# Kernel tuning notes

Hardware: AMD Instinct MI355X
Metric: run time of the kernel (lower is better)

The kernel has to match this reference:

```python
import jax, jax.numpy as jnp
import numpy as np

B, T, N, D, H, E = 64, 64, 32, 32, 128, 256


def setup_inputs() -> dict:
    key = jax.random.key(0)
    ks = jax.random.split(key, 20)

    def g(k, shape, scale=0.1):
        return (jax.random.normal(k, shape, dtype=jnp.float32) * scale)

    return {
        "ts_batch": jax.random.normal(ks[0], (B, T, N, D), dtype=jnp.float32),
        "edge_index": jax.random.randint(ks[1], (2, E), 0, N, dtype=jnp.int32),
        # encoder: 2-layer GCN-LSTM, gates packed as [i,f,g,o] -> 4H
        "Wen0": g(ks[2], (D + H, 4 * H)), "ben0": jnp.zeros((4 * H,), jnp.float32),
        "Wen1": g(ks[3], (2 * H, 4 * H)), "ben1": jnp.zeros((4 * H,), jnp.float32),
        # decoder: 2-layer GCN-LSTM
        "Wde0": g(ks[4], (D + H, 4 * H)), "bde0": jnp.zeros((4 * H,), jnp.float32),
        "Wde1": g(ks[5], (2 * H, 4 * H)), "bde1": jnp.zeros((4 * H,), jnp.float32),
        # per-node linears (the nn.ModuleList loops, batched as [N, in, out])
        "Wmu": g(ks[6], (N, H, H)), "bmu": jnp.zeros((N, H), jnp.float32),
        "Wlv": g(ks[7], (N, H, H)), "blv": jnp.zeros((N, H), jnp.float32),
        "Who": g(ks[8], (N, H, D)), "bho": jnp.zeros((N, D), jnp.float32),
        "Wholv": g(ks[9], (N, H, D)), "bholv": jnp.zeros((N, D), jnp.float32),
        # reparametrization noise (torch.randn_like), made explicit for determinism
        "eps": jax.random.normal(ks[10], (B, N, H), dtype=jnp.float32),
    }


def reference(ts_batch, edge_index, Wen0, ben0, Wen1, ben1, Wde0, bde0, Wde1, bde1,
              Wmu, bmu, Wlv, blv, Who, bho, Wholv, bholv, eps):
    n = Wmu.shape[0]
    # GCN normalized adjacency with self-loops: D^{-1/2}(A+I)D^{-1/2}
    A = jnp.zeros((n, n), jnp.float32).at[edge_index[1], edge_index[0]].add(1.0)
    A = A + jnp.eye(n, dtype=jnp.float32)
    dinv = jax.lax.rsqrt(A.sum(axis=1))
    A = dinv[:, None] * A * dinv[None, :]

    def gcn(x, W, b):  # x: [B,N,F] -> [B,N,4H]
        return jnp.einsum('ij,bjf->bif', A, x) @ W + b

    def cell(x, h, c, W, b):
        z = gcn(jnp.concatenate([x, h], axis=-1), W, b)
        i, f, g, o = jnp.split(z, 4, axis=-1)
        c = jax.nn.sigmoid(f) * c + jax.nn.sigmoid(i) * jnp.tanh(g)
        h = jax.nn.sigmoid(o) * jnp.tanh(c)
        return h, c

    def pnl(x, W, b):  # per-node linear, replaces the python loop over ModuleList
        return jnp.einsum('bnh,nho->bno', x, W) + b

    bsz, tlen = ts_batch.shape[0], ts_batch.shape[1]
    hdim = Wen0.shape[1] // 4
    z0 = jnp.zeros((bsz, n, hdim), jnp.float32)

    def enc_step(carry, x_t):
        h0, c0, h1, c1 = carry
        h0, c0 = cell(x_t, h0, c0, Wen0, ben0)
        h1, c1 = cell(h0, h1, c1, Wen1, ben1)
        return (h0, c0, h1, c1), None

    (h0, c0, h1, c1), _ = jax.lax.scan(
        enc_step, (z0, z0, z0, z0), jnp.transpose(ts_batch, (1, 0, 2, 3)))

    mu = pnl(h1, Wmu, bmu)
    logvar = pnl(h1, Wlv, blv)
    zlat = mu + eps * jnp.exp(logvar)  # reparametrize (note: exp(logvar), as in source)

    out_last = pnl(zlat, Who, bho)
    outlv_last = pnl(zlat, Wholv, bholv)

    # decoder initialized from encoder final (pre-reparam) hidden state; runs in
    # reverse time feeding back its own output (inference / no teacher forcing)
    def dec_step(carry, _):
        h0, c0, h1, c1, prev = carry
        h0, c0 = cell(prev, h0, c0, Wde0, bde0)
        h1, c1 = cell(h0, h1, c1, Wde1, bde1)
        out = pnl(h1, Who, bho)
        outlv = pnl(h1, Wholv, bholv)
        return (h0, c0, h1, c1, out), (out, outlv)

    _, (outs, outlvs) = jax.lax.scan(
        dec_step, (h0, c0, h1, c1, out_last), None, length=tlen - 1)

    # outs are for timesteps T-2 .. 0; reverse and append step T-1
    output = jnp.concatenate([outs[::-1], out_last[None]], axis=0)
    output_logvar = jnp.concatenate([outlvs[::-1], outlv_last[None]], axis=0)
    output = jnp.transpose(output, (1, 0, 2, 3))            # [B,T,N,D]
    output_logvar = jnp.transpose(output_logvar, (1, 0, 2, 3))
    return output, zlat, mu, logvar, output_logvar
```

## Files before the change

kernel.cpp:

```cpp
#include <hip/hip_runtime.h>


typedef unsigned short u16;
typedef unsigned int u32;
typedef short bf16x8 __attribute__((ext_vector_type(8)));
typedef float f32x4 __attribute__((ext_vector_type(4)));

#define O_OUT 0
#define O_Z   4194304
#define O_MU  4456448
#define O_LV  4718592
#define O_OLV 4980736

#define WS_ABF  0
#define WS_PEN0 1280
#define WS_PEN1 83200
#define WS_PDE0 214272
#define WS_PDE1 296192
#define WS_PHO  427264
#define WS_PLV  558336
#define WS_H1   689408
#define WS_NEED_BYTES 34408960ull

#define XSTR 552

__device__ __forceinline__ u16 f2b(float f){
  unsigned x = __float_as_uint(f);
  x += 0x7fffu + ((x>>16)&1u);
  return (u16)(x>>16);
}
__device__ __forceinline__ float b2f(u16 u){ return __uint_as_float(((unsigned)u)<<16); }
__device__ __forceinline__ float blo(unsigned u){ return __uint_as_float(u<<16); }
__device__ __forceinline__ float bhi(unsigned u){ return __uint_as_float(u & 0xffff0000u); }

__device__ __forceinline__ float rcp_(float x){ return __builtin_amdgcn_rcpf(x); }
__device__ __forceinline__ float sigm(float x){ return rcp_(1.f + __expf(-x)); }
__device__ __forceinline__ float tanh_(float x){
  float e = __expf(-2.f*fabsf(x));
  float r = (1.f - e) * rcp_(1.f + e);
  return __builtin_copysignf(r, x);
}

__global__ void adj_kernel(const int* __restrict__ ei, u16* __restrict__ ws)
{
  __shared__ float As[1024];
  __shared__ float dinv[32];
  const int tid = threadIdx.x;
  for (int e = tid; e < 1024; e += 256) As[e] = 0.f;
  __syncthreads();
  atomicAdd(&As[ei[256 + tid]*32 + ei[tid]], 1.f);
  __syncthreads();
  if (tid < 32) As[tid*33] += 1.f;
  __syncthreads();
  if (tid < 32){
    float s = 0.f;
    for (int j=0;j<32;++j) s += As[tid*32 + j];
    dinv[tid] = rsqrtf(s);
  }
  __syncthreads();
  for (int e = tid; e < 1280; e += 256){
    int i = e / 40, j = e % 40;
    float v = (j < 32) ? As[i*32 + j]*dinv[i]*dinv[j] : 0.f;
    ws[WS_ABF + e] = f2b(v);
  }
}

__global__ void pack_kernel(const float* __restrict__ Wen0, const float* __restrict__ Wen1,
                            const float* __restrict__ Wde0, const float* __restrict__ Wde1,
                            const float* __restrict__ Who,  const float* __restrict__ Wholv,
                            u16* __restrict__ ws)
{
  int id = blockIdx.x*256 + threadIdx.x;
  if (id < 53248){
    const float* W; int KS, dstoff, lid;
    if (id < 10240){ W = Wen0; KS = 5; dstoff = WS_PEN0; lid = id; }
    else if (id < 26624){ W = Wen1; KS = 8; dstoff = WS_PEN1; lid = id - 10240; }
    else if (id < 36864){ W = Wde0; KS = 5; dstoff = WS_PDE0; lid = id - 26624; }
    else { W = Wde1; KS = 8; dstoff = WS_PDE1; lid = id - 36864; }
    int l = lid & 63, rest = lid >> 6;
    int ks = rest % KS, nt = rest / KS;
    int n  = nt*16 + (l & 15);
    int k0 = ks*32 + (l >> 4)*8;
    u16 tmp[8];
    #pragma unroll
    for (int j=0;j<8;++j) tmp[j] = f2b(W[(k0 + j)*512 + n]);
    uint4 v;
    v.x = (unsigned)tmp[0] | ((unsigned)tmp[1] << 16);
    v.y = (unsigned)tmp[2] | ((unsigned)tmp[3] << 16);
    v.z = (unsigned)tmp[4] | ((unsigned)tmp[5] << 16);
    v.w = (unsigned)tmp[6] | ((unsigned)tmp[7] << 16);
    *(uint4*)&ws[dstoff + lid*8] = v;
  } else {
    int e = id - 53248;
    const float* src = (e < 16384) ? Who : Wholv;
    int dsto = (e < 16384) ? WS_PHO : WS_PLV;
    e &= 16383;
    int n = e >> 9, r = e & 511;
    int d = r >> 4, h0 = (r & 15)*8;
    u16 tmp[8];
    #pragma unroll
    for (int j=0;j<8;++j) tmp[j] = f2b(src[(n*128 + h0 + j)*32 + d]);
    uint4 v;
    v.x = (unsigned)tmp[0] | ((unsigned)tmp[1] << 16);
    v.y = (unsigned)tmp[2] | ((unsigned)tmp[3] << 16);
    v.z = (unsigned)tmp[4] | ((unsigned)tmp[5] << 16);
    v.w = (unsigned)tmp[6] | ((unsigned)tmp[7] << 16);
    *(uint4*)&ws[dsto + (n*4096 + d*128 + h0)] = v;
  }
}

template<int KS>
__device__ __forceinline__ void cell_tail(
    f32x4 (&acc)[2][4], const float* bias4,
    u16* XN, u16* yt,
    const bf16x8 afr0, const bf16x8 afr1,
    f32x4 (&cst)[2], int hwrite, int l15, int lq, int wave)
{
  f32x4 acc2[2][4];
  u32* yt32 = (u32*)yt;
  #pragma unroll
  for (int hh=0; hh<2; ++hh){
    #pragma unroll
    for (int g2=0; g2<2; ++g2){
      const int g = hh*2 + g2;
      #pragma unroll
      for (int mt=0; mt<2; ++mt){
        u32 lo = (u32)f2b(acc[mt][g][0]) | ((u32)f2b(acc[mt][g][1]) << 16);
        u32 hi = (u32)f2b(acc[mt][g][2]) | ((u32)f2b(acc[mt][g][3]) << 16);
        const int base = (g2*16 + l15)*20 + mt*8 + lq*2;
        yt32[base]     = lo;
        yt32[base + 1] = hi;
      }
    }
    #pragma unroll
    for (int g2=0; g2<2; ++g2){
      const int g = hh*2 + g2;
      bf16x8 bfr = *(const bf16x8*)&yt[(g2*16 + l15)*40 + lq*8];
      f32x4 vb = {bias4[g], bias4[g], bias4[g], bias4[g]};
      acc2[0][g] = __builtin_amdgcn_mfma_f32_16x16x32_bf16(afr0, bfr, vb, 0, 0, 0);
      acc2[1][g] = __builtin_amdgcn_mfma_f32_16x16x32_bf16(afr1, bfr, vb, 0, 0, 0);
    }
  }
  const int col = wave*16 + l15;
  #pragma unroll
  for (int mt=0;mt<2;++mt){
    #pragma unroll
    for (int q=0;q<4;++q){
      float iv = sigm(acc2[mt][0][q]);
      float fv = sigm(acc2[mt][1][q]);
      float gv = tanh_(acc2[mt][2][q]);
      float ov = sigm(acc2[mt][3][q]);
      float c  = fv*cst[mt][q] + iv*gv;
      cst[mt][q] = c;
      float h  = ov*tanh_(c);
      XN[(mt*16 + lq*4 + q)*XSTR + hwrite + col] = f2b(h);
    }
  }
}

template<int KS, int N0>
__device__ __forceinline__ void run_cell_jit(
    const u16* __restrict__ PW, const float* bias4,
    u16* XN, u16* yt,
    const bf16x8 afr0, const bf16x8 afr1,
    f32x4 (&cst)[2], int kb0, int kb1, int hwrite,
    int l15, int lq, int wave)
{
  const bf16x8* PW8 = (const bf16x8*)PW;
  const int lane = lq*16 + l15;
  f32x4 acc[2][4];
  #pragma unroll
  for (int mt=0;mt<2;++mt)
    #pragma unroll
    for (int g=0;g<4;++g){ f32x4 z = {0.f,0.f,0.f,0.f}; acc[mt][g] = z; }
  #pragma unroll
  for (int ks=0; ks<KS; ++ks){
    const int off = (ks < N0) ? (kb0 + ks*32) : (kb1 + (ks - N0)*32);
    bf16x8 a0 = *(const bf16x8*)&XN[l15*XSTR + off + lq*8];
    bf16x8 a1 = *(const bf16x8*)&XN[(16 + l15)*XSTR + off + lq*8];
    #pragma unroll
    for (int g=0; g<4; ++g){
      bf16x8 bwf = PW8[((g*8 + wave)*KS + ks)*64 + lane];
      acc[0][g] = __builtin_amdgcn_mfma_f32_16x16x32_bf16(a0, bwf, acc[0][g], 0, 0, 0);
      acc[1][g] = __builtin_amdgcn_mfma_f32_16x16x32_bf16(a1, bwf, acc[1][g], 0, 0, 0);
    }
  }
  cell_tail<KS>(acc, bias4, XN, yt, afr0, afr1, cst, hwrite, l15, lq, wave);
}

template<int KS, int N0>
__device__ __forceinline__ void run_cell_res(
    const bf16x8 (&bw)[8][4], const float* bias4,
    u16* XN, u16* yt,
    const bf16x8 afr0, const bf16x8 afr1,
    f32x4 (&cst)[2], int kb0, int kb1, int hwrite,
    int l15, int lq, int wave)
{
  f32x4 acc[2][4];
  #pragma unroll
  for (int mt=0;mt<2;++mt)
    #pragma unroll
    for (int g=0;g<4;++g){ f32x4 z = {0.f,0.f,0.f,0.f}; acc[mt][g] = z; }
  #pragma unroll
  for (int ks=0; ks<KS; ++ks){
    const int off = (ks < N0) ? (kb0 + ks*32) : (kb1 + (ks - N0)*32);
    bf16x8 a0 = *(const bf16x8*)&XN[l15*XSTR + off + lq*8];
    bf16x8 a1 = *(const bf16x8*)&XN[(16 + l15)*XSTR + off + lq*8];
    #pragma unroll
    for (int g=0; g<4; ++g){
      acc[0][g] = __builtin_amdgcn_mfma_f32_16x16x32_bf16(a0, bw[ks][g], acc[0][g], 0, 0, 0);
      acc[1][g] = __builtin_amdgcn_mfma_f32_16x16x32_bf16(a1, bw[ks][g], acc[1][g], 0, 0, 0);
    }
  }
  cell_tail<KS>(acc, bias4, XN, yt, afr0, afr1, cst, hwrite, l15, lq, wave);
}

template<bool SAVE>
__global__ __launch_bounds__(512, 2) void lstm_main(
  const float* __restrict__ ts,
  const float* __restrict__ ben0, const float* __restrict__ ben1,
  const float* __restrict__ bde0, const float* __restrict__ bde1,
  const float* __restrict__ Wmu, const float* __restrict__ bmu,
  const float* __restrict__ Wlv, const float* __restrict__ blv,
  const float* __restrict__ bho, const float* __restrict__ bholv,
  const float* __restrict__ Wholv,
  const float* __restrict__ eps,
  const u16* __restrict__ ws, u16* __restrict__ wsH1,
  float* __restrict__ dout)
{
  __shared__ __align__(16) u16 XN[32*XSTR];
  __shared__ __align__(16) u16 Abf[32*40];
  __shared__ __align__(16) u16 Ytr[8*32*40];
  float* zl = (float*)Ytr;

  const int tid  = threadIdx.x;
  const int lane = tid & 63, wave = tid >> 6;
  const int l15  = lane & 15, lq = lane >> 4;
  const int b    = blockIdx.x;
  u16* yt = Ytr + wave*(32*40);

  for (int e = tid; e < 1280;     e += 512) Abf[e] = ws[WS_ABF + e];
  for (int e = tid; e < 32*XSTR;  e += 512) XN[e] = 0;
  f32x4 c0[2], c1[2];
  {
    f32x4 zz = {0.f,0.f,0.f,0.f};
    c0[0]=c0[1]=c1[0]=c1[1]=zz;
  }
  float biE0[4], biE1[4], biD0[4], biD1[4];
  const int colg = wave*16 + l15;
  #pragma unroll
  for (int g=0; g<4; ++g){
    biE0[g] = ben0[g*128+colg];
    biE1[g] = ben1[g*128+colg];
    biD0[g] = bde0[g*128+colg];
    biD1[g] = bde1[g*128+colg];
  }
  const u16* whoT = ws + WS_PHO;
  const u16* wlvT = ws + WS_PLV;
  __syncthreads();
  const bf16x8 afr0 = *(const bf16x8*)&Abf[l15*40 + lq*8];
  const bf16x8 afr1 = *(const bf16x8*)&Abf[(16 + l15)*40 + lq*8];
  {
    const float* xp = ts + (size_t)(b*64)*1024;
    for (int e = tid; e < 1024; e += 512)
      XN[(e >> 5)*XSTR + (e & 31)] = f2b(xp[e]);
  }
  bf16x8 bw1[8][4];
  {
    const bf16x8* PW8 = (const bf16x8*)(ws + WS_PEN1);
    #pragma unroll
    for (int ks=0; ks<8; ++ks)
      #pragma unroll
      for (int g=0; g<4; ++g)
        bw1[ks][g] = PW8[((g*8 + wave)*8 + ks)*64 + lane];
  }
  __syncthreads();

  for (int t=0; t<64; ++t){
    const int ph = t & 1;
    run_cell_jit<5,1>(ws+WS_PEN0, biE0, XN, yt, afr0, afr1, c0,
                      0, 32 + 128*ph, 32 + 128*(1-ph), l15, lq, wave);
    __syncthreads();
    if (t < 63){
      const float* xp = ts + (size_t)(b*64 + t + 1)*1024;
      for (int e = tid; e < 1024; e += 512)
        XN[(e >> 5)*XSTR + (e & 31)] = f2b(xp[e]);
    }
    run_cell_res<8,4>(bw1, biE1, XN, yt, afr0, afr1, c1,
                      32 + 128*(1-ph), 288 + 128*ph, 288 + 128*(1-ph), l15, lq, wave);
    __syncthreads();
  }

  for (int k=0;k<8;++k){
    int idx = tid + k*512;
    int n = idx >> 7, o = idx & 127;
    float am = bmu[idx];
    float al = blv[idx];
    for (int h=0; h<128; ++h){
      float hv = b2f(XN[n*XSTR + 288 + h]);
      am += hv * Wmu[(n*128 + h)*128 + o];
      al += hv * Wlv[(n*128 + h)*128 + o];
    }
    float zv = am + eps[b*4096 + idx] * __expf(al);
    zl[idx] = zv;
    dout[O_MU + b*4096 + idx] = am;
    dout[O_LV + b*4096 + idx] = al;
    dout[O_Z  + b*4096 + idx] = zv;
  }
  __syncthreads();
  #pragma unroll
  for (int k=0;k<2;++k){
    int idx = tid + k*512;
    int n = idx >> 5, d = idx & 31;
    float a  = bho[idx];
    float a2 = bholv[idx];
    const u16* wp = whoT + (idx << 7);
    for (int h=0; h<128; ++h){
      float hv = zl[n*128 + h];
      a  += hv * b2f(wp[h]);
      a2 += hv * Wholv[(n*128+h)*32 + d];
    }
    dout[O_OUT + (size_t)(b*64 + 63)*1024 + idx] = a;
    dout[O_OLV + (size_t)(b*64 + 63)*1024 + idx] = a2;
    XN[n*XSTR + d] = f2b(a);
  }
  {
    const bf16x8* PW8 = (const bf16x8*)(ws + WS_PDE1);
    #pragma unroll
    for (int ks=0; ks<8; ++ks)
      #pragma unroll
      for (int g=0; g<4; ++g)
        bw1[ks][g] = PW8[((g*8 + wave)*8 + ks)*64 + lane];
  }
  __syncthreads();

  for (int s=0; s<63; ++s){
    const int pg = s & 1;
    run_cell_jit<5,1>(ws+WS_PDE0, biD0, XN, yt, afr0, afr1, c0,
                      0, 32 + 128*pg, 32 + 128*(1-pg), l15, lq, wave);
    __syncthreads();
    run_cell_res<8,4>(bw1, biD1, XN, yt, afr0, afr1, c1,
                      32 + 128*(1-pg), 288 + 128*pg, 288 + 128*(1-pg), l15, lq, wave);
    __syncthreads();
    const int h1b = 288 + 128*(1-pg);
    if (SAVE){
      u16* dst = wsH1 + (size_t)(b*63 + s)*4096;
      for (int k=0;k<8;++k){
        int idx = tid + k*512;
        dst[idx] = XN[(idx >> 7)*XSTR + h1b + (idx & 127)];
      }
    }
    const int tt = 62 - s;
    #pragma unroll
    for (int k=0;k<2;++k){
      int idx = tid + k*512;
      int n = idx >> 5, d = idx & 31;
      float a = bho[idx];
      const u16* wp = whoT + (idx << 7);
      if (SAVE){
        #pragma unroll 4
        for (int h=0; h<128; h+=8){
          uint4 hv = *(const uint4*)&XN[n*XSTR + h1b + h];
          uint4 wv = *(const uint4*)&wp[h];
          a += blo(hv.x)*blo(wv.x) + bhi(hv.x)*bhi(wv.x);
          a += blo(hv.y)*blo(wv.y) + bhi(hv.y)*bhi(wv.y);
          a += blo(hv.z)*blo(wv.z) + bhi(hv.z)*bhi(wv.z);
          a += blo(hv.w)*blo(wv.w) + bhi(hv.w)*bhi(wv.w);
        }
      } else {
        float a2 = bholv[idx];
        const u16* wp2 = wlvT + (idx << 7);
        #pragma unroll 4
        for (int h=0; h<128; h+=8){
          uint4 hv = *(const uint4*)&XN[n*XSTR + h1b + h];
          uint4 wv = *(const uint4*)&wp[h];
          uint4 w2 = *(const uint4*)&wp2[h];
          float s0=blo(hv.x), s1=bhi(hv.x), s2=blo(hv.y), s3=bhi(hv.y);
          float s4=blo(hv.z), s5=bhi(hv.z), s6=blo(hv.w), s7=bhi(hv.w);
          a  += s0*blo(wv.x) + s1*bhi(wv.x) + s2*blo(wv.y) + s3*bhi(wv.y)
              + s4*blo(wv.z) + s5*bhi(wv.z) + s6*blo(wv.w) + s7*bhi(wv.w);
          a2 += s0*blo(w2.x) + s1*bhi(w2.x) + s2*blo(w2.y) + s3*bhi(w2.y)
              + s4*blo(w2.z) + s5*bhi(w2.z) + s6*blo(w2.w) + s7*bhi(w2.w);
        }
        dout[O_OLV + (size_t)(b*64 + tt)*1024 + idx] = a2;
      }
      dout[O_OUT + (size_t)(b*64 + tt)*1024 + idx] = a;
      XN[n*XSTR + d] = f2b(a);
    }
    __syncthreads();
  }
}

__global__ __launch_bounds__(256) void outlv_kernel(
    const u16* __restrict__ wsH1, const u16* __restrict__ ws,
    const float* __restrict__ bholv, float* __restrict__ dout)
{
  const int n = blockIdx.x, t = blockIdx.y, tid = threadIdx.x;
  __shared__ __align__(16) u16 Ls[64*128];
  const int s = 62 - t;
  for (int e = tid; e < 8192; e += 256){
    int b = e >> 7;
    Ls[e] = wsH1[(size_t)(b*63 + s)*4096 + n*128 + (e & 127)];
  }
  __syncthreads();
  const int d = tid & 31, bq = tid >> 5;
  const u16* wp2 = ws + WS_PLV + ((n*32 + d) << 7);
  const float bias = bholv[n*32 + d];
  for (int b = bq; b < 64; b += 8){
    float acc = bias;
    #pragma unroll 4
    for (int h = 0; h < 128; h += 8){
      uint4 sv = *(const uint4*)&Ls[b*128 + h];
      uint4 wv = *(const uint4*)&wp2[h];
      acc += blo(sv.x)*blo(wv.x) + bhi(sv.x)*bhi(wv.x);
      acc += blo(sv.y)*blo(wv.y) + bhi(sv.y)*bhi(wv.y);
      acc += blo(sv.z)*blo(wv.z) + bhi(sv.z)*bhi(wv.z);
      acc += blo(sv.w)*blo(wv.w) + bhi(sv.w)*bhi(wv.w);
    }
    dout[O_OLV + (size_t)(b*64 + t)*1024 + n*32 + d] = acc;
  }
}

extern "C" void kernel_launch(void* const* d_in, const int* in_sizes, int n_in,
                              void* d_out, int out_size, void* d_ws, size_t ws_size,
                              hipStream_t stream)
{
  (void)in_sizes; (void)n_in; (void)out_size;
  const float* ts   = (const float*)d_in[0];
  const int*   ei   = (const int*)d_in[1];
  const float* Wen0 = (const float*)d_in[2];
  const float* ben0 = (const float*)d_in[3];
  const float* Wen1 = (const float*)d_in[4];
  const float* ben1 = (const float*)d_in[5];
  const float* Wde0 = (const float*)d_in[6];
  const float* bde0 = (const float*)d_in[7];
  const float* Wde1 = (const float*)d_in[8];
  const float* bde1 = (const float*)d_in[9];
  const float* Wmu  = (const float*)d_in[10];
  const float* bmu  = (const float*)d_in[11];
  const float* Wlv  = (const float*)d_in[12];
  const float* blv  = (const float*)d_in[13];
  const float* Who  = (const float*)d_in[14];
  const float* bho  = (const float*)d_in[15];
  const float* Wholv= (const float*)d_in[16];
  const float* bholv= (const float*)d_in[17];
  const float* eps  = (const float*)d_in[18];
  u16*   ws   = (u16*)d_ws;
  float* dout = (float*)d_out;
  const bool save = ws_size >= WS_NEED_BYTES;

  adj_kernel<<<1, 256, 0, stream>>>(ei, ws);
  pack_kernel<<<336, 256, 0, stream>>>(Wen0, Wen1, Wde0, Wde1, Who, Wholv, ws);
  if (save){
    lstm_main<true><<<64, 512, 0, stream>>>(ts, ben0, ben1, bde0, bde1, Wmu, bmu, Wlv, blv,
        bho, bholv, Wholv, eps, ws, ws + WS_H1, dout);
    outlv_kernel<<<dim3(32,63), 256, 0, stream>>>(ws + WS_H1, ws, bholv, dout);
  } else {
    lstm_main<false><<<64, 512, 0, stream>>>(ts, ben0, ben1, bde0, bde1, Wmu, bmu, Wlv, blv,
        bho, bholv, Wholv, eps, ws, ws, dout);
  }
}
```

Baseline: 1.923 ms.

## Widen LDS buffers, restructure cell tail, hoist weight loads and vectorize H1 save

Several independent tweaks land together. The XN row stride grows to 936 and the per-wave transpose scratch doubles, so the cell tail can write all four gates with 64-bit stores before running its MFMAs, instead of two half-passes. tanh switches to a shorter exp2-based formula, each k-step's four JIT weight fragments are loaded before its MFMAs, and the encoder layer-1 register weights are loaded before the first barrier. The H1 save becomes one 16-byte copy per thread instead of eight scalar copies. The larger LDS footprint may limit the two-blocks-per-CU target, and the new tanh is less accurate for large inputs.

```diff
diff --git a/kernel.cpp b/kernel.cpp
--- a/kernel.cpp
+++ b/kernel.cpp
@@ -22,7 +22,7 @@
 #define WS_H1   689408
 #define WS_NEED_BYTES 34408960ull
 
-#define XSTR 552
+#define XSTR 936
 
 __device__ __forceinline__ u16 f2b(float f){
   unsigned x = __float_as_uint(f);
@@ -36,9 +36,8 @@
 __device__ __forceinline__ float rcp_(float x){ return __builtin_amdgcn_rcpf(x); }
 __device__ __forceinline__ float sigm(float x){ return rcp_(1.f + __expf(-x)); }
 __device__ __forceinline__ float tanh_(float x){
-  float e = __expf(-2.f*fabsf(x));
-  float r = (1.f - e) * rcp_(1.f + e);
-  return __builtin_copysignf(r, x);
+  float e = __builtin_amdgcn_exp2f(2.8853900817779268f * x);
+  return 1.f - 2.f*rcp_(e + 1.f);
 }
 
 __global__ void adj_kernel(const int* __restrict__ ei, u16* __restrict__ ws)
@@ -109,7 +108,6 @@
   }
 }
 
-template<int KS>
 __device__ __forceinline__ void cell_tail(
     f32x4 (&acc)[2][4], const float* bias4,
     u16* XN, u16* yt,
@@ -119,27 +117,22 @@
   f32x4 acc2[2][4];
   u32* yt32 = (u32*)yt;
   #pragma unroll
-  for (int hh=0; hh<2; ++hh){
-    #pragma unroll
-    for (int g2=0; g2<2; ++g2){
-      const int g = hh*2 + g2;
-      #pragma unroll
-      for (int mt=0; mt<2; ++mt){
-        u32 lo = (u32)f2b(acc[mt][g][0]) | ((u32)f2b(acc[mt][g][1]) << 16);
-        u32 hi = (u32)f2b(acc[mt][g][2]) | ((u32)f2b(acc[mt][g][3]) << 16);
-        const int base = (g2*16 + l15)*20 + mt*8 + lq*2;
-        yt32[base]     = lo;
-        yt32[base + 1] = hi;
-      }
-    }
-    #pragma unroll
-    for (int g2=0; g2<2; ++g2){
-      const int g = hh*2 + g2;
-      bf16x8 bfr = *(const bf16x8*)&yt[(g2*16 + l15)*40 + lq*8];
-      f32x4 vb = {bias4[g], bias4[g], bias4[g], bias4[g]};
-      acc2[0][g] = __builtin_amdgcn_mfma_f32_16x16x32_bf16(afr0, bfr, vb, 0, 0, 0);
-      acc2[1][g] = __builtin_amdgcn_mfma_f32_16x16x32_bf16(afr1, bfr, vb, 0, 0, 0);
-    }
+  for (int g=0; g<4; ++g){
+    #pragma unroll
+    for (int mt=0; mt<2; ++mt){
+      u32 lo = (u32)f2b(acc[mt][g][0]) | ((u32)f2b(acc[mt][g][1]) << 16);
+      u32 hi = (u32)f2b(acc[mt][g][2]) | ((u32)f2b(acc[mt][g][3]) << 16);
+      const int base = (g*16 + l15)*20 + mt*8 + lq*2;
+      uint2 v; v.x = lo; v.y = hi;
+      *(uint2*)&yt32[base] = v;
+    }
+  }
+  #pragma unroll
+  for (int g=0; g<4; ++g){
+    bf16x8 bfr = *(const bf16x8*)&yt[(g*16 + l15)*40 + lq*8];
+    f32x4 vb = {bias4[g], bias4[g], bias4[g], bias4[g]};
+    acc2[0][g] = __builtin_amdgcn_mfma_f32_16x16x32_bf16(afr0, bfr, vb, 0, 0, 0);
+    acc2[1][g] = __builtin_amdgcn_mfma_f32_16x16x32_bf16(afr1, bfr, vb, 0, 0, 0);
   }
   const int col = wave*16 + l15;
   #pragma unroll
@@ -160,7 +153,7 @@
 
 template<int KS, int N0>
 __device__ __forceinline__ void run_cell_jit(
-    const u16* __restrict__ PW, const float* bias4,
+    const u16* PW, const float* bias4,
     u16* XN, u16* yt,
     const bf16x8 afr0, const bf16x8 afr1,
     f32x4 (&cst)[2], int kb0, int kb1, int hwrite,
@@ -175,17 +168,20 @@
     for (int g=0;g<4;++g){ f32x4 z = {0.f,0.f,0.f,0.f}; acc[mt][g] = z; }
   #pragma unroll
   for (int ks=0; ks<KS; ++ks){
+    bf16x8 bw[4];
+    #pragma unroll
+    for (int g=0; g<4; ++g)
+      bw[g] = PW8[((g*8 + wave)*KS + ks)*64 + lane];
     const int off = (ks < N0) ? (kb0 + ks*32) : (kb1 + (ks - N0)*32);
     bf16x8 a0 = *(const bf16x8*)&XN[l15*XSTR + off + lq*8];
     bf16x8 a1 = *(const bf16x8*)&XN[(16 + l15)*XSTR + off + lq*8];
     #pragma unroll
     for (int g=0; g<4; ++g){
-      bf16x8 bwf = PW8[((g*8 + wave)*KS + ks)*64 + lane];
-      acc[0][g] = __builtin_amdgcn_mfma_f32_16x16x32_bf16(a0, bwf, acc[0][g], 0, 0, 0);
-      acc[1][g] = __builtin_amdgcn_mfma_f32_16x16x32_bf16(a1, bwf, acc[1][g], 0, 0, 0);
-    }
-  }
-  cell_tail<KS>(acc, bias4, XN, yt, afr0, afr1, cst, hwrite, l15, lq, wave);
+      acc[0][g] = __builtin_amdgcn_mfma_f32_16x16x32_bf16(a0, bw[g], acc[0][g], 0, 0, 0);
+      acc[1][g] = __builtin_amdgcn_mfma_f32_16x16x32_bf16(a1, bw[g], acc[1][g], 0, 0, 0);
+    }
+  }
+  cell_tail(acc, bias4, XN, yt, afr0, afr1, cst, hwrite, l15, lq, wave);
 }
 
 template<int KS, int N0>
@@ -212,7 +208,7 @@
       acc[1][g] = __builtin_amdgcn_mfma_f32_16x16x32_bf16(a1, bw[ks][g], acc[1][g], 0, 0, 0);
     }
   }
-  cell_tail<KS>(acc, bias4, XN, yt, afr0, afr1, cst, hwrite, l15, lq, wave);
+  cell_tail(acc, bias4, XN, yt, afr0, afr1, cst, hwrite, l15, lq, wave);
 }
 
 template<bool SAVE>
@@ -225,19 +221,19 @@
   const float* __restrict__ bho, const float* __restrict__ bholv,
   const float* __restrict__ Wholv,
   const float* __restrict__ eps,
-  const u16* __restrict__ ws, u16* __restrict__ wsH1,
+  u16* ws, u16* __restrict__ wsH1,
   float* __restrict__ dout)
 {
   __shared__ __align__(16) u16 XN[32*XSTR];
   __shared__ __align__(16) u16 Abf[32*40];
-  __shared__ __align__(16) u16 Ytr[8*32*40];
+  __shared__ __align__(16) u16 Ytr[8*64*40];
   float* zl = (float*)Ytr;
 
   const int tid  = threadIdx.x;
   const int lane = tid & 63, wave = tid >> 6;
   const int l15  = lane & 15, lq = lane >> 4;
   const int b    = blockIdx.x;
-  u16* yt = Ytr + wave*(32*40);
+  u16* yt = Ytr + wave*(64*40);
 
   for (int e = tid; e < 1280;     e += 512) Abf[e] = ws[WS_ABF + e];
   for (int e = tid; e < 32*XSTR;  e += 512) XN[e] = 0;
@@ -257,6 +253,16 @@
   }
   const u16* whoT = ws + WS_PHO;
   const u16* wlvT = ws + WS_PLV;
+  const int lane_ = lq*16 + l15;
+  bf16x8 bw1[8][4];
+  {
+    const bf16x8* PW8 = (const bf16x8*)(ws + WS_PEN1);
+    #pragma unroll
+    for (int ks=0; ks<8; ++ks)
+      #pragma unroll
+      for (int g=0; g<4; ++g)
+        bw1[ks][g] = PW8[((g*8 + wave)*8 + ks)*64 + lane_];
+  }
   __syncthreads();
   const bf16x8 afr0 = *(const bf16x8*)&Abf[l15*40 + lq*8];
   const bf16x8 afr1 = *(const bf16x8*)&Abf[(16 + l15)*40 + lq*8];
@@ -264,15 +270,6 @@
     const float* xp = ts + (size_t)(b*64)*1024;
     for (int e = tid; e < 1024; e += 512)
       XN[(e >> 5)*XSTR + (e & 31)] = f2b(xp[e]);
-  }
-  bf16x8 bw1[8][4];
-  {
-    const bf16x8* PW8 = (const bf16x8*)(ws + WS_PEN1);
-    #pragma unroll
-    for (int ks=0; ks<8; ++ks)
-      #pragma unroll
-      for (int g=0; g<4; ++g)
-        bw1[ks][g] = PW8[((g*8 + wave)*8 + ks)*64 + lane];
   }
   __syncthreads();
 
@@ -330,7 +327,7 @@
     for (int ks=0; ks<8; ++ks)
       #pragma unroll
       for (int g=0; g<4; ++g)
-        bw1[ks][g] = PW8[((g*8 + wave)*8 + ks)*64 + lane];
+        bw1[ks][g] = PW8[((g*8 + wave)*8 + ks)*64 + lane_];
   }
   __syncthreads();
 
@@ -345,10 +342,9 @@
     const int h1b = 288 + 128*(1-pg);
     if (SAVE){
       u16* dst = wsH1 + (size_t)(b*63 + s)*4096;
-      for (int k=0;k<8;++k){
-        int idx = tid + k*512;
-        dst[idx] = XN[(idx >> 7)*XSTR + h1b + (idx & 127)];
-      }
+      int idx = tid*8;
+      int n = idx >> 7, h = idx & 127;
+      *(uint4*)&dst[idx] = *(const uint4*)&XN[n*XSTR + h1b + h];
     }
     const int tt = 62 - s;
     #pragma unroll
```

Measured after the change: 1.821 ms. 5.3% less time.
